# Kernel optimization log

Measured on AMD Instinct MI355X. Metric: run time of the kernel, lower is better.

## Reference

```python
import jax, jax.numpy as jnp
import numpy as np

B, CH, H, W = 32, 128, 32, 32
EMB = 64      # embedding_dim
NEMB = 8192   # codebook size


def setup_inputs() -> dict:
    key = jax.random.key(0)
    k1, k2, k3, k4 = jax.random.split(key, 4)
    z = jax.random.normal(k1, (B, CH, H, W), jnp.float32)
    # 1x1 conv == per-pixel linear: weight [EMB, CH], bias [EMB]
    proj_w = jax.random.normal(k2, (EMB, CH), jnp.float32) * 0.05
    proj_b = jax.random.normal(k3, (EMB,), jnp.float32) * 0.01
    embed_w = jax.random.normal(k4, (NEMB, EMB), jnp.float32)
    return {"z": z, "proj_w": proj_w, "proj_b": proj_b, "embed_w": embed_w}


def reference(z, proj_w, proj_b, embed_w):
    Bz, C, Hh, Ww = z.shape
    sg = jax.lax.stop_gradient
    # 1x1 conv then permute(0,2,3,1): [B,C,H,W] -> [B,H,W,E]
    z_e = jnp.einsum('bchw,ec->bhwe', z, proj_w) + proj_b
    flat = z_e.reshape(-1, z_e.shape[-1])  # [N, E], N = B*H*W
    dist = ((flat * flat).sum(1, keepdims=True)
            - 2.0 * (flat @ embed_w.T)
            + (embed_w * embed_w).sum(1)[None, :])
    z_q_ind = jnp.argmin(dist, axis=1).reshape(Bz, Hh, Ww)  # argmax(-dist)
    z_q_emb = embed_w[z_q_ind]  # gather: [B,H,W,E]
    commitment_cost = 0.25
    kld_scale = 10.0
    latent_loss = kld_scale * (
        commitment_cost * jnp.mean((sg(z_q_emb) - z_e) ** 2)
        + jnp.mean((z_q_emb - sg(z_e)) ** 2))
    z_q_flat = z_q_emb
    # straight-through estimator
    z_q_st = z_e + sg(z_q_emb - z_e)
    out = jnp.transpose(z_q_st, (0, 3, 1, 2))  # [B,E,H,W]
    return out, z_q_flat, latent_loss, z_q_ind
```

## Files before the change

kernel.cpp:

```cpp
#include <hip/hip_runtime.h>

#define NPIX   32768
#define NEMB_  8192
#define EMB_   64
#define CH_    128
#define CAPP   768

#define OUT_OFF  0
#define ZQ_OFF   2097152
#define LOSS_OFF 4194304
#define IND_OFF  4194305

typedef _Float16 h8   __attribute__((ext_vector_type(8)));
typedef float    f16f __attribute__((ext_vector_type(16)));

__global__ __launch_bounds__(256) void k_wpack(
    const float* __restrict__ ew, const float* __restrict__ pw,
    float4* __restrict__ W4, float* __restrict__ pwT,
    float* __restrict__ wsq, float* __restrict__ wsqp,
    float* __restrict__ lacc, int* __restrict__ done)
{
    const int tid = threadIdx.x;
    {
        const int i = blockIdx.x * 256 + tid;
        const float v = pw[i];
        const int e = i >> 7, c = i & 127;
        pwT[c * 64 + e] = v;
    }
    const int m = blockIdx.x * 256 + tid;
    const float4* wr = (const float4*)(ew + (size_t)m * EMB_);
    float w[EMB_];
    float s = 0.f;
    #pragma unroll
    for (int i = 0; i < 16; i++) {
        float4 v = wr[i];
        w[4*i] = v.x; w[4*i+1] = v.y; w[4*i+2] = v.z; w[4*i+3] = v.w;
        s += v.x*v.x + v.y*v.y + v.z*v.z + v.w*v.w;
    }
    wsq[m] = s;
    float sh = (float)(_Float16)s;
    float sl = s - sh;
    const int t  = m >> 5;
    const int li = m & 31;
    #pragma unroll
    for (int s5 = 0; s5 < 4; s5++) {
        #pragma unroll
        for (int h = 0; h < 2; h++) {
            h8 hh;
            #pragma unroll
            for (int j = 0; j < 8; j++) hh[j] = (_Float16)w[s5 * 16 + h * 8 + j];
            W4[(size_t)(t * 5 + s5) * 64 + h * 32 + li] = __builtin_bit_cast(float4, hh);
        }
    }
    {
        h8 hh;
        #pragma unroll
        for (int j = 0; j < 8; j++) hh[j] = (_Float16)0.f;
        hh[0] = (_Float16)sh; hh[1] = (_Float16)sl;
        W4[(size_t)(t * 5 + 4) * 64 + 0 * 32 + li] = __builtin_bit_cast(float4, hh);
        #pragma unroll
        for (int j = 0; j < 8; j++) hh[j] = (_Float16)0.f;
        W4[(size_t)(t * 5 + 4) * 64 + 1 * 32 + li] = __builtin_bit_cast(float4, hh);
    }
    __shared__ float red[256];
    red[tid] = s;
    __syncthreads();
    for (int o = 128; o > 0; o >>= 1) {
        if (tid < o) red[tid] = fmaxf(red[tid], red[tid + o]);
        __syncthreads();
    }
    if (tid == 0) wsqp[blockIdx.x] = red[0];
    if (blockIdx.x == 0 && tid == 0) { *lacc = 0.f; *done = 0; }
}

__global__ __launch_bounds__(256) void k_proj(
    const float* __restrict__ z, const float* __restrict__ pwT,
    const float* __restrict__ pb, float* __restrict__ z_e,
    float* __restrict__ xsq)
{
    __shared__ float xp[4][64];
    const int tid  = threadIdx.x;
    const int px   = tid & 63;
    const int eqv  = tid >> 6;
    const int eq16 = __builtin_amdgcn_readfirstlane(eqv << 4);
    const int n  = blockIdx.x * 64 + px;
    const int b  = n >> 10;
    const int hw = n & 1023;
    const float* zp = z + (size_t)b * (CH_ * 1024) + hw;

    float acc[16];
    #pragma unroll
    for (int j = 0; j < 16; j++) acc[j] = 0.f;

    #pragma unroll 4
    for (int c = 0; c < CH_; c++) {
        const float zv = zp[(size_t)c * 1024];
        const float4* wr = (const float4*)(pwT + c * 64 + eq16);
        float4 w0 = wr[0], w1 = wr[1], w2 = wr[2], w3 = wr[3];
        acc[0]  = fmaf(zv, w0.x, acc[0]);  acc[1]  = fmaf(zv, w0.y, acc[1]);
        acc[2]  = fmaf(zv, w0.z, acc[2]);  acc[3]  = fmaf(zv, w0.w, acc[3]);
        acc[4]  = fmaf(zv, w1.x, acc[4]);  acc[5]  = fmaf(zv, w1.y, acc[5]);
        acc[6]  = fmaf(zv, w1.z, acc[6]);  acc[7]  = fmaf(zv, w1.w, acc[7]);
        acc[8]  = fmaf(zv, w2.x, acc[8]);  acc[9]  = fmaf(zv, w2.y, acc[9]);
        acc[10] = fmaf(zv, w2.z, acc[10]); acc[11] = fmaf(zv, w2.w, acc[11]);
        acc[12] = fmaf(zv, w3.x, acc[12]); acc[13] = fmaf(zv, w3.y, acc[13]);
        acc[14] = fmaf(zv, w3.z, acc[14]); acc[15] = fmaf(zv, w3.w, acc[15]);
    }

    const float4* pb4 = (const float4*)(pb + eq16);
    float4 b0 = pb4[0], b1 = pb4[1], b2 = pb4[2], b3 = pb4[3];
    float bb[16] = {b0.x,b0.y,b0.z,b0.w, b1.x,b1.y,b1.z,b1.w,
                    b2.x,b2.y,b2.z,b2.w, b3.x,b3.y,b3.z,b3.w};
    float sq = 0.f;
    #pragma unroll
    for (int j = 0; j < 16; j++) { acc[j] += bb[j]; sq += acc[j] * acc[j]; }

    float4* zo = (float4*)(z_e + (size_t)n * EMB_ + eq16);
    zo[0] = make_float4(acc[0],  acc[1],  acc[2],  acc[3]);
    zo[1] = make_float4(acc[4],  acc[5],  acc[6],  acc[7]);
    zo[2] = make_float4(acc[8],  acc[9],  acc[10], acc[11]);
    zo[3] = make_float4(acc[12], acc[13], acc[14], acc[15]);
    xp[eqv][px] = sq;
    __syncthreads();
    if (tid < 64)
        xsq[blockIdx.x * 64 + tid] = xp[0][tid] + xp[1][tid] + xp[2][tid] + xp[3][tid];
}

__device__ __forceinline__ unsigned long long pack_key(float d, int m)
{
    unsigned fb = __float_as_uint(d);
    fb ^= ((int)fb < 0) ? 0xFFFFFFFFu : 0x80000000u;
    return ((unsigned long long)fb << 32) | (unsigned)m;
}

__global__ __launch_bounds__(512, 2) void k_fused3(
    const float4* __restrict__ W4, const float* __restrict__ z_e,
    const float* __restrict__ xsq, const float* __restrict__ wsqp,
    const float* __restrict__ wsq, const float* __restrict__ ew,
    float* __restrict__ out, float* __restrict__ lacc, int* __restrict__ done)
{
    __shared__ __align__(16) float xs[128][68];
    __shared__ float s1s[1024], s2s[1024], s3s[1024];
    __shared__ short i1s[1024], i2s[1024];
    __shared__ float thr_s[128];
    __shared__ int   pairs[CAPP];
    __shared__ unsigned long long pbest[128];
    __shared__ int   winner_s[128];
    __shared__ int   smask[128];
    __shared__ float wred[8];
    __shared__ int   npair_s;
    __shared__ float wm_s;

    const int tid  = threadIdx.x;
    const int wv   = tid >> 6;
    const int lane = tid & 63;
    const int n0   = blockIdx.x * 128;
    const int hlf  = lane >> 5;

    if (tid == 0) npair_s = 0;
    if (tid < 128) { smask[tid] = 0; pbest[tid] = ~0ULL; }
    if (tid < 32) {
        float w = wsqp[tid];
        #pragma unroll
        for (int o = 16; o > 0; o >>= 1) w = fmaxf(w, __shfl_xor(w, o));
        if (tid == 0) wm_s = w;
    }
    #pragma unroll
    for (int k = 0; k < 4; k++) {
        const int idx = k * 512 + tid;
        const int px = idx >> 4, i = idx & 15;
        ((float4*)&xs[px][0])[i] =
            *(const float4*)(z_e + (size_t)(n0 + px) * EMB_ + i * 4);
    }
    __syncthreads();

    h8 bfr[4][5];
    #pragma unroll
    for (int j = 0; j < 4; j++) {
        const int px = j * 32 + (lane & 31);
        #pragma unroll
        for (int s5 = 0; s5 < 4; s5++) {
            float4 u0 = *(const float4*)(&xs[px][s5 * 16 + hlf * 8]);
            float4 u1 = *(const float4*)(&xs[px][s5 * 16 + hlf * 8 + 4]);
            h8 hh;
            hh[0]=(_Float16)u0.x; hh[1]=(_Float16)u0.y; hh[2]=(_Float16)u0.z; hh[3]=(_Float16)u0.w;
            hh[4]=(_Float16)u1.x; hh[5]=(_Float16)u1.y; hh[6]=(_Float16)u1.z; hh[7]=(_Float16)u1.w;
            bfr[j][s5] = hh;
        }
        h8 hh;
        #pragma unroll
        for (int q = 0; q < 8; q++) hh[q] = (_Float16)0.f;
        if (hlf == 0) { hh[0] = (_Float16)-0.5f; hh[1] = (_Float16)-0.5f; }
        bfr[j][4] = hh;
    }

    const f16f kzero = {0,0,0,0,0,0,0,0,0,0,0,0,0,0,0,0};
    float s1[4], s2[4], s3[4];
    int   i1[4], i2[4];
    #pragma unroll
    for (int j = 0; j < 4; j++) { s1[j]=s2[j]=s3[j]=-3.0e38f; i1[j]=i2[j]=0; }

    const int tb = wv * 32;
    const float4* Wb = W4 + (size_t)tb * 320 + lane;
    float4 A0[5], A1[5];
    #pragma unroll
    for (int s = 0; s < 5; s++) A0[s] = Wb[s * 64];
    #pragma unroll
    for (int s = 0; s < 5; s++) A1[s] = Wb[320 + s * 64];

#define TILE_BODY(AB, TT, PF)                                                  \
    {                                                                          \
        const int gt = tb + (TT);                                              \
        f16f acc[4];                                                           \
        _Pragma("unroll")                                                      \
        for (int j = 0; j < 4; j++)                                            \
            acc[j] = __builtin_amdgcn_mfma_f32_32x32x16_f16(                   \
                __builtin_bit_cast(h8, AB[0]), bfr[j][0], kzero, 0, 0, 0);     \
        _Pragma("unroll")                                                      \
        for (int s = 1; s < 5; s++) {                                          \
            h8 a = __builtin_bit_cast(h8, AB[s]);                              \
            _Pragma("unroll")                                                  \
            for (int j = 0; j < 4; j++)                                        \
                acc[j] = __builtin_amdgcn_mfma_f32_32x32x16_f16(a, bfr[j][s],  \
                                                                acc[j],0,0,0); \
        }                                                                      \
        {                                                                      \
            const int tp = (PF) < 32 ? (PF) : 31;                              \
            const float4* wp = Wb + (size_t)tp * 320;                          \
            _Pragma("unroll")                                                  \
            for (int s = 0; s < 5; s++) AB[s] = wp[s * 64];                    \
        }                                                                      \
        _Pragma("unroll")                                                      \
        for (int j = 0; j < 4; j++) {                                          \
            float t0 = fmaxf(fmaxf(acc[j][0],  acc[j][1]),  acc[j][2]);        \
            float t1 = fmaxf(fmaxf(acc[j][3],  acc[j][4]),  acc[j][5]);        \
            float t2 = fmaxf(fmaxf(acc[j][6],  acc[j][7]),  acc[j][8]);        \
            float t3 = fmaxf(fmaxf(acc[j][9],  acc[j][10]), acc[j][11]);       \
            float t4 = fmaxf(fmaxf(acc[j][12], acc[j][13]), acc[j][14]);       \
            float v  = fmaxf(fmaxf(fmaxf(t0, t1), fmaxf(t2, t3)),              \
                             fmaxf(t4, acc[j][15]));                           \
            v = fmaxf(v, __shfl_xor(v, 32));                                   \
            bool c1 = v > s1[j];                                               \
            bool c2 = v > s2[j];                                               \
            int  cand = c1 ? i1[j] : gt;                                       \
            i2[j] = c2 ? cand : i2[j];                                         \
            s3[j] = fmaxf(fminf(s2[j], v), s3[j]);                             \
            s3[j] = fminf(s3[j], fmaxf(s2[j], v));                             \
            s2[j] = fmaxf(fminf(s1[j], v), fminf(s2[j], fmaxf(s1[j], v)));     \
            i1[j] = c1 ? gt : i1[j];                                           \
            s1[j] = fmaxf(s1[j], v);                                           \
        }                                                                      \
    }

    for (int tt = 0; tt < 32; tt += 2) {
        TILE_BODY(A0, tt,     tt + 2)
        TILE_BODY(A1, tt + 1, tt + 3)
    }
#undef TILE_BODY

    if (lane < 32) {
        #pragma unroll
        for (int j = 0; j < 4; j++) {
            const int cell = (j * 32 + lane) * 8 + wv;
            s1s[cell] = s1[j]; s2s[cell] = s2[j]; s3s[cell] = s3[j];
            i1s[cell] = (short)i1[j]; i2s[cell] = (short)i2[j];
        }
    }
    __syncthreads();

    if (tid < 128) {
        float s1g = s1s[tid * 8];
        #pragma unroll
        for (int c = 1; c < 8; c++) s1g = fmaxf(s1g, s1s[tid * 8 + c]);
        float E = 0.00125f * sqrtf(xsq[n0 + tid] * wm_s) + 1e-5f * wm_s + 3e-4f;
        thr_s[tid] = s1g - 2.0f * E;
    }
    __syncthreads();
    #pragma unroll
    for (int k = 0; k < 2; k++) {
        const int cell = k * 512 + tid;
        const int px = cell >> 3, ch = cell & 7;
        const float th = thr_s[px];
        const float cs1 = s1s[cell], cs2 = s2s[cell], cs3 = s3s[cell];
        if (cs3 >= th) {
            int pos = atomicAdd(&npair_s, 32);
            if (pos + 32 <= CAPP) {
                for (int t = 0; t < 32; t++)
                    pairs[pos + t] = (px << 8) | (ch * 32 + t);
            } else {
                for (int t = 0; t < 32; t++)
                    if (pos + t < CAPP) pairs[pos + t] = -1;
                smask[px] = 1;
            }
        } else {
            if (cs1 >= th) {
                int pos = atomicAdd(&npair_s, 1);
                if (pos < CAPP) pairs[pos] = (px << 8) | (int)i1s[cell];
                else smask[px] = 1;
            }
            if (cs2 >= th) {
                int pos = atomicAdd(&npair_s, 1);
                if (pos < CAPP) pairs[pos] = (px << 8) | (int)i2s[cell];
                else smask[px] = 1;
            }
        }
    }
    __syncthreads();
    const int np = npair_s < CAPP ? npair_s : CAPP;

    const int lg = lane >> 4;
    const int ld = lane & 15;
    for (int i = wv; i < np; i += 8) {
        const int pr = pairs[i];
        if (pr < 0) continue;
        const int p = pr >> 8;
        if (smask[p]) continue;
        const int t = pr & 255;
        const float4* tb4 = (const float4*)(ew + (size_t)t * 2048);
        float4 wq[8];
        #pragma unroll
        for (int q = 0; q < 8; q++) wq[q] = tb4[q * 64 + lane];
        const float4 xq = *(const float4*)(&xs[p][ld * 4]);
        unsigned long long best = ~0ULL;
        #pragma unroll
        for (int q = 0; q < 8; q++) {
            float dp = wq[q].x*xq.x + wq[q].y*xq.y + wq[q].z*xq.z + wq[q].w*xq.w;
            dp += __shfl_xor(dp, 1);
            dp += __shfl_xor(dp, 2);
            dp += __shfl_xor(dp, 4);
            dp += __shfl_xor(dp, 8);
            const int m = t * 32 + q * 4 + lg;
            unsigned long long key = pack_key(fmaf(-2.f, dp, wsq[m]), m);
            best = key < best ? key : best;
        }
        { unsigned long long o = __shfl_xor(best, 16); best = o < best ? o : best; }
        { unsigned long long o = __shfl_xor(best, 32); best = o < best ? o : best; }
        if (lane == 0) atomicMin(&pbest[p], best);
    }
    for (int p = wv; p < 128; p += 8) {
        if (!smask[p]) continue;
        const float4 xq = *(const float4*)(&xs[p][ld * 4]);
        unsigned long long bk = ~0ULL;
        for (int t = 0; t < 256; t++) {
            const float4* tb4 = (const float4*)(ew + (size_t)t * 2048);
            #pragma unroll
            for (int q = 0; q < 8; q++) {
                float4 wv4 = tb4[q * 64 + lane];
                float dp = wv4.x*xq.x + wv4.y*xq.y + wv4.z*xq.z + wv4.w*xq.w;
                dp += __shfl_xor(dp, 1);
                dp += __shfl_xor(dp, 2);
                dp += __shfl_xor(dp, 4);
                dp += __shfl_xor(dp, 8);
                const int m = t * 32 + q * 4 + lg;
                unsigned long long key = pack_key(fmaf(-2.f, dp, wsq[m]), m);
                bk = key < bk ? key : bk;
            }
        }
        { unsigned long long o = __shfl_xor(bk, 16); bk = o < bk ? o : bk; }
        { unsigned long long o = __shfl_xor(bk, 32); bk = o < bk ? o : bk; }
        if (lane == 0) atomicMin(&pbest[p], bk);
    }
    __syncthreads();
    if (tid < 128) {
        const int win = (int)(unsigned)(pbest[tid] & 0xFFFFFFFFULL);
        winner_s[tid] = win;
        out[IND_OFF + n0 + tid] = (float)win;
    }
    __syncthreads();
    float lsum = 0.f;
    {
        const int px = tid >> 2, sg = tid & 3;
        const int win = winner_s[px];
        const float4* wr = (const float4*)(ew + (size_t)win * EMB_ + sg * 16);
        float4* xr  = (float4*)(&xs[px][sg * 16]);
        float4* zq4 = (float4*)(out + ZQ_OFF + (size_t)(n0 + px) * EMB_ + sg * 16);
        #pragma unroll
        for (int i = 0; i < 4; i++) {
            float4 w4v = wr[i];
            float4 z4  = xr[i];
            float d0 = w4v.x - z4.x, d1 = w4v.y - z4.y;
            float d2 = w4v.z - z4.z, d3 = w4v.w - z4.w;
            lsum += d0*d0 + d1*d1 + d2*d2 + d3*d3;
            xr[i]  = w4v;
            zq4[i] = w4v;
        }
    }
    __syncthreads();
    {
        const int bI  = n0 >> 10;
        const int hw0 = n0 & 1023;
        float* ob = out + OUT_OFF + (size_t)bI * (EMB_ * 1024) + hw0;
        #pragma unroll
        for (int r = 0; r < 16; r++) {
            const int idx = r * 512 + tid;
            const int e = idx >> 7, px = idx & 127;
            ob[(size_t)e * 1024 + px] = xs[px][e];
        }
    }
    {
        float v = lsum;
        #pragma unroll
        for (int o = 1; o < 64; o <<= 1) v += __shfl_xor(v, o);
        if (lane == 0) wred[wv] = v;
    }
    __syncthreads();
    if (tid == 0) {
        float s = wred[0];
        #pragma unroll
        for (int k = 1; k < 8; k++) s += wred[k];
        atomicAdd(lacc, s);
        __threadfence();
        int old = atomicAdd(done, 1);
        if (old == (int)gridDim.x - 1) {
            float tot = atomicAdd(lacc, 0.0f);
            out[LOSS_OFF] = 12.5f * (tot / 2097152.0f);
        }
    }
}

extern "C" void kernel_launch(void* const* d_in, const int* in_sizes, int n_in,
                              void* d_out, int out_size, void* d_ws, size_t ws_size,
                              hipStream_t stream)
{
    const float* z  = (const float*)d_in[0];
    const float* pw = (const float*)d_in[1];
    const float* pb = (const float*)d_in[2];
    const float* ew = (const float*)d_in[3];
    float* out = (float*)d_out;

    char* ws = (char*)d_ws;
    float4* W4   = (float4*)(ws);
    float*  pwT  = (float*) (ws + 1310720);
    float*  xsq  = (float*) (ws + 1343488);
    float*  wsq  = (float*) (ws + 1474560);
    float*  wsqp = (float*) (ws + 1507328);
    float*  lacc = (float*) (ws + 1507456);
    int*    done = (int*)   (ws + 1507460);

    float* z_e = out + ZQ_OFF;

    hipLaunchKernelGGL(k_wpack,  dim3(32),  dim3(256), 0, stream,
                       ew, pw, W4, pwT, wsq, wsqp, lacc, done);
    hipLaunchKernelGGL(k_proj,   dim3(512), dim3(256), 0, stream,
                       z, pwT, pb, z_e, xsq);
    hipLaunchKernelGGL(k_fused3, dim3(256), dim3(512), 0, stream,
                       W4, z_e, xsq, wsqp, wsq, ew, out, lacc, done);
}
```

Baseline: 174.2 us.

## Fuse 1x1 projection into the VQ kernel and double threads per block

```diff
diff --git a/kernel.cpp b/kernel.cpp
--- a/kernel.cpp
+++ b/kernel.cpp
@@ -73,59 +73,6 @@
     if (blockIdx.x == 0 && tid == 0) { *lacc = 0.f; *done = 0; }
 }
 
-__global__ __launch_bounds__(256) void k_proj(
-    const float* __restrict__ z, const float* __restrict__ pwT,
-    const float* __restrict__ pb, float* __restrict__ z_e,
-    float* __restrict__ xsq)
-{
-    __shared__ float xp[4][64];
-    const int tid  = threadIdx.x;
-    const int px   = tid & 63;
-    const int eqv  = tid >> 6;
-    const int eq16 = __builtin_amdgcn_readfirstlane(eqv << 4);
-    const int n  = blockIdx.x * 64 + px;
-    const int b  = n >> 10;
-    const int hw = n & 1023;
-    const float* zp = z + (size_t)b * (CH_ * 1024) + hw;
-
-    float acc[16];
-    #pragma unroll
-    for (int j = 0; j < 16; j++) acc[j] = 0.f;
-
-    #pragma unroll 4
-    for (int c = 0; c < CH_; c++) {
-        const float zv = zp[(size_t)c * 1024];
-        const float4* wr = (const float4*)(pwT + c * 64 + eq16);
-        float4 w0 = wr[0], w1 = wr[1], w2 = wr[2], w3 = wr[3];
-        acc[0]  = fmaf(zv, w0.x, acc[0]);  acc[1]  = fmaf(zv, w0.y, acc[1]);
-        acc[2]  = fmaf(zv, w0.z, acc[2]);  acc[3]  = fmaf(zv, w0.w, acc[3]);
-        acc[4]  = fmaf(zv, w1.x, acc[4]);  acc[5]  = fmaf(zv, w1.y, acc[5]);
-        acc[6]  = fmaf(zv, w1.z, acc[6]);  acc[7]  = fmaf(zv, w1.w, acc[7]);
-        acc[8]  = fmaf(zv, w2.x, acc[8]);  acc[9]  = fmaf(zv, w2.y, acc[9]);
-        acc[10] = fmaf(zv, w2.z, acc[10]); acc[11] = fmaf(zv, w2.w, acc[11]);
-        acc[12] = fmaf(zv, w3.x, acc[12]); acc[13] = fmaf(zv, w3.y, acc[13]);
-        acc[14] = fmaf(zv, w3.z, acc[14]); acc[15] = fmaf(zv, w3.w, acc[15]);
-    }
-
-    const float4* pb4 = (const float4*)(pb + eq16);
-    float4 b0 = pb4[0], b1 = pb4[1], b2 = pb4[2], b3 = pb4[3];
-    float bb[16] = {b0.x,b0.y,b0.z,b0.w, b1.x,b1.y,b1.z,b1.w,
-                    b2.x,b2.y,b2.z,b2.w, b3.x,b3.y,b3.z,b3.w};
-    float sq = 0.f;
-    #pragma unroll
-    for (int j = 0; j < 16; j++) { acc[j] += bb[j]; sq += acc[j] * acc[j]; }
-
-    float4* zo = (float4*)(z_e + (size_t)n * EMB_ + eq16);
-    zo[0] = make_float4(acc[0],  acc[1],  acc[2],  acc[3]);
-    zo[1] = make_float4(acc[4],  acc[5],  acc[6],  acc[7]);
-    zo[2] = make_float4(acc[8],  acc[9],  acc[10], acc[11]);
-    zo[3] = make_float4(acc[12], acc[13], acc[14], acc[15]);
-    xp[eqv][px] = sq;
-    __syncthreads();
-    if (tid < 64)
-        xsq[blockIdx.x * 64 + tid] = xp[0][tid] + xp[1][tid] + xp[2][tid] + xp[3][tid];
-}
-
 __device__ __forceinline__ unsigned long long pack_key(float d, int m)
 {
     unsigned fb = __float_as_uint(d);
@@ -133,21 +80,23 @@
     return ((unsigned long long)fb << 32) | (unsigned)m;
 }
 
-__global__ __launch_bounds__(512, 2) void k_fused3(
-    const float4* __restrict__ W4, const float* __restrict__ z_e,
-    const float* __restrict__ xsq, const float* __restrict__ wsqp,
-    const float* __restrict__ wsq, const float* __restrict__ ew,
+__global__ __launch_bounds__(1024, 4) void k_fused3(
+    const float4* __restrict__ W4, const float* __restrict__ z,
+    const float* __restrict__ pwT, const float* __restrict__ pb,
+    const float* __restrict__ wsqp, const float* __restrict__ wsq,
+    const float* __restrict__ ew,
     float* __restrict__ out, float* __restrict__ lacc, int* __restrict__ done)
 {
     __shared__ __align__(16) float xs[128][68];
-    __shared__ float s1s[1024], s2s[1024], s3s[1024];
-    __shared__ short i1s[1024], i2s[1024];
+    __shared__ float s1s[2048], s2s[2048], s3s[2048];
+    __shared__ short i1s[2048], i2s[2048];
+    __shared__ float xsqp_s[8][128];
     __shared__ float thr_s[128];
     __shared__ int   pairs[CAPP];
     __shared__ unsigned long long pbest[128];
     __shared__ int   winner_s[128];
     __shared__ int   smask[128];
-    __shared__ float wred[8];
+    __shared__ float wred[16];
     __shared__ int   npair_s;
     __shared__ float wm_s;
 
@@ -165,12 +114,35 @@
         for (int o = 16; o > 0; o >>= 1) w = fmaxf(w, __shfl_xor(w, o));
         if (tid == 0) wm_s = w;
     }
-    #pragma unroll
-    for (int k = 0; k < 4; k++) {
-        const int idx = k * 512 + tid;
-        const int px = idx >> 4, i = idx & 15;
-        ((float4*)&xs[px][0])[i] =
-            *(const float4*)(z_e + (size_t)(n0 + px) * EMB_ + i * 4);
+
+    {
+        const int oct = tid >> 7;
+        const int pxp = tid & 127;
+        const int e0  = __builtin_amdgcn_readfirstlane(oct << 3);
+        const float* zp = z + (size_t)(n0 >> 10) * (CH_ * 1024) + (n0 & 1023) + pxp;
+        float acc[8];
+        #pragma unroll
+        for (int j = 0; j < 8; j++) acc[j] = 0.f;
+        #pragma unroll 8
+        for (int c = 0; c < CH_; c++) {
+            const float zv = zp[(size_t)c * 1024];
+            const float4* wr = (const float4*)(pwT + c * 64 + e0);
+            float4 w0 = wr[0], w1 = wr[1];
+            acc[0] = fmaf(zv, w0.x, acc[0]); acc[1] = fmaf(zv, w0.y, acc[1]);
+            acc[2] = fmaf(zv, w0.z, acc[2]); acc[3] = fmaf(zv, w0.w, acc[3]);
+            acc[4] = fmaf(zv, w1.x, acc[4]); acc[5] = fmaf(zv, w1.y, acc[5]);
+            acc[6] = fmaf(zv, w1.z, acc[6]); acc[7] = fmaf(zv, w1.w, acc[7]);
+        }
+        const float4* pb4 = (const float4*)(pb + e0);
+        float4 b0 = pb4[0], b1 = pb4[1];
+        acc[0] += b0.x; acc[1] += b0.y; acc[2] += b0.z; acc[3] += b0.w;
+        acc[4] += b1.x; acc[5] += b1.y; acc[6] += b1.z; acc[7] += b1.w;
+        float sq = 0.f;
+        #pragma unroll
+        for (int j = 0; j < 8; j++) sq += acc[j] * acc[j];
+        ((float4*)&xs[pxp][0])[oct * 2]     = make_float4(acc[0], acc[1], acc[2], acc[3]);
+        ((float4*)&xs[pxp][0])[oct * 2 + 1] = make_float4(acc[4], acc[5], acc[6], acc[7]);
+        xsqp_s[oct][pxp] = sq;
     }
     __syncthreads();
 
@@ -200,68 +172,72 @@
     #pragma unroll
     for (int j = 0; j < 4; j++) { s1[j]=s2[j]=s3[j]=-3.0e38f; i1[j]=i2[j]=0; }
 
-    const int tb = wv * 32;
+    const int tb = wv * 16;
     const float4* Wb = W4 + (size_t)tb * 320 + lane;
-    float4 A0[5], A1[5];
-    #pragma unroll
-    for (int s = 0; s < 5; s++) A0[s] = Wb[s * 64];
-    #pragma unroll
-    for (int s = 0; s < 5; s++) A1[s] = Wb[320 + s * 64];
-
-#define TILE_BODY(AB, TT, PF)                                                  \
+    float4 A[5];
+    #pragma unroll
+    for (int s = 0; s < 5; s++) A[s] = Wb[s * 64];
+
+#define REDUCE_J(ACC, JJ)                                                      \
     {                                                                          \
-        const int gt = tb + (TT);                                              \
-        f16f acc[4];                                                           \
-        _Pragma("unroll")                                                      \
-        for (int j = 0; j < 4; j++)                                            \
-            acc[j] = __builtin_amdgcn_mfma_f32_32x32x16_f16(                   \
-                __builtin_bit_cast(h8, AB[0]), bfr[j][0], kzero, 0, 0, 0);     \
-        _Pragma("unroll")                                                      \
-        for (int s = 1; s < 5; s++) {                                          \
-            h8 a = __builtin_bit_cast(h8, AB[s]);                              \
-            _Pragma("unroll")                                                  \
-            for (int j = 0; j < 4; j++)                                        \
-                acc[j] = __builtin_amdgcn_mfma_f32_32x32x16_f16(a, bfr[j][s],  \
-                                                                acc[j],0,0,0); \
-        }                                                                      \
-        {                                                                      \
-            const int tp = (PF) < 32 ? (PF) : 31;                              \
-            const float4* wp = Wb + (size_t)tp * 320;                          \
-            _Pragma("unroll")                                                  \
-            for (int s = 0; s < 5; s++) AB[s] = wp[s * 64];                    \
-        }                                                                      \
-        _Pragma("unroll")                                                      \
-        for (int j = 0; j < 4; j++) {                                          \
-            float t0 = fmaxf(fmaxf(acc[j][0],  acc[j][1]),  acc[j][2]);        \
-            float t1 = fmaxf(fmaxf(acc[j][3],  acc[j][4]),  acc[j][5]);        \
-            float t2 = fmaxf(fmaxf(acc[j][6],  acc[j][7]),  acc[j][8]);        \
-            float t3 = fmaxf(fmaxf(acc[j][9],  acc[j][10]), acc[j][11]);       \
-            float t4 = fmaxf(fmaxf(acc[j][12], acc[j][13]), acc[j][14]);       \
-            float v  = fmaxf(fmaxf(fmaxf(t0, t1), fmaxf(t2, t3)),              \
-                             fmaxf(t4, acc[j][15]));                           \
-            v = fmaxf(v, __shfl_xor(v, 32));                                   \
-            bool c1 = v > s1[j];                                               \
-            bool c2 = v > s2[j];                                               \
-            int  cand = c1 ? i1[j] : gt;                                       \
-            i2[j] = c2 ? cand : i2[j];                                         \
-            s3[j] = fmaxf(fminf(s2[j], v), s3[j]);                             \
-            s3[j] = fminf(s3[j], fmaxf(s2[j], v));                             \
-            s2[j] = fmaxf(fminf(s1[j], v), fminf(s2[j], fmaxf(s1[j], v)));     \
-            i1[j] = c1 ? gt : i1[j];                                           \
-            s1[j] = fmaxf(s1[j], v);                                           \
-        }                                                                      \
-    }
-
-    for (int tt = 0; tt < 32; tt += 2) {
-        TILE_BODY(A0, tt,     tt + 2)
-        TILE_BODY(A1, tt + 1, tt + 3)
-    }
-#undef TILE_BODY
+        float t0 = fmaxf(fmaxf(ACC[0],  ACC[1]),  ACC[2]);                     \
+        float t1 = fmaxf(fmaxf(ACC[3],  ACC[4]),  ACC[5]);                     \
+        float t2 = fmaxf(fmaxf(ACC[6],  ACC[7]),  ACC[8]);                     \
+        float t3 = fmaxf(fmaxf(ACC[9],  ACC[10]), ACC[11]);                    \
+        float t4 = fmaxf(fmaxf(ACC[12], ACC[13]), ACC[14]);                    \
+        float v  = fmaxf(fmaxf(fmaxf(t0, t1), fmaxf(t2, t3)),                  \
+                         fmaxf(t4, ACC[15]));                                  \
+        v = fmaxf(v, __shfl_xor(v, 32));                                       \
+        bool c1 = v > s1[JJ];                                                  \
+        bool c2 = v > s2[JJ];                                                  \
+        int  cand = c1 ? i1[JJ] : gt;                                          \
+        i2[JJ] = c2 ? cand : i2[JJ];                                           \
+        s3[JJ] = fmaxf(fminf(s2[JJ], v), s3[JJ]);                              \
+        s3[JJ] = fminf(s3[JJ], fmaxf(s2[JJ], v));                              \
+        s2[JJ] = fmaxf(fminf(s1[JJ], v), fminf(s2[JJ], fmaxf(s1[JJ], v)));     \
+        i1[JJ] = c1 ? gt : i1[JJ];                                             \
+        s1[JJ] = fmaxf(s1[JJ], v);                                             \
+    }
+
+    for (int tt = 0; tt < 16; tt++) {
+        const int gt = tb + tt;
+        f16f acc0 = __builtin_amdgcn_mfma_f32_32x32x16_f16(
+            __builtin_bit_cast(h8, A[0]), bfr[0][0], kzero, 0, 0, 0);
+        f16f acc1 = __builtin_amdgcn_mfma_f32_32x32x16_f16(
+            __builtin_bit_cast(h8, A[0]), bfr[1][0], kzero, 0, 0, 0);
+        #pragma unroll
+        for (int s = 1; s < 5; s++) {
+            h8 a = __builtin_bit_cast(h8, A[s]);
+            acc0 = __builtin_amdgcn_mfma_f32_32x32x16_f16(a, bfr[0][s], acc0, 0, 0, 0);
+            acc1 = __builtin_amdgcn_mfma_f32_32x32x16_f16(a, bfr[1][s], acc1, 0, 0, 0);
+        }
+        REDUCE_J(acc0, 0)
+        REDUCE_J(acc1, 1)
+        f16f acc2 = __builtin_amdgcn_mfma_f32_32x32x16_f16(
+            __builtin_bit_cast(h8, A[0]), bfr[2][0], kzero, 0, 0, 0);
+        f16f acc3 = __builtin_amdgcn_mfma_f32_32x32x16_f16(
+            __builtin_bit_cast(h8, A[0]), bfr[3][0], kzero, 0, 0, 0);
+        #pragma unroll
+        for (int s = 1; s < 5; s++) {
+            h8 a = __builtin_bit_cast(h8, A[s]);
+            acc2 = __builtin_amdgcn_mfma_f32_32x32x16_f16(a, bfr[2][s], acc2, 0, 0, 0);
+            acc3 = __builtin_amdgcn_mfma_f32_32x32x16_f16(a, bfr[3][s], acc3, 0, 0, 0);
+        }
+        {
+            const int tp = (tt + 1) < 16 ? (tt + 1) : 15;
+            const float4* wp = Wb + (size_t)tp * 320;
+            #pragma unroll
+            for (int s = 0; s < 5; s++) A[s] = wp[s * 64];
+        }
+        REDUCE_J(acc2, 2)
+        REDUCE_J(acc3, 3)
+    }
+#undef REDUCE_J
 
     if (lane < 32) {
         #pragma unroll
         for (int j = 0; j < 4; j++) {
-            const int cell = (j * 32 + lane) * 8 + wv;
+            const int cell = (j * 32 + lane) * 16 + wv;
             s1s[cell] = s1[j]; s2s[cell] = s2[j]; s3s[cell] = s3[j];
             i1s[cell] = (short)i1[j]; i2s[cell] = (short)i2[j];
         }
@@ -269,26 +245,29 @@
     __syncthreads();
 
     if (tid < 128) {
-        float s1g = s1s[tid * 8];
-        #pragma unroll
-        for (int c = 1; c < 8; c++) s1g = fmaxf(s1g, s1s[tid * 8 + c]);
-        float E = 0.00125f * sqrtf(xsq[n0 + tid] * wm_s) + 1e-5f * wm_s + 3e-4f;
+        float s1g = s1s[tid * 16];
+        #pragma unroll
+        for (int c = 1; c < 16; c++) s1g = fmaxf(s1g, s1s[tid * 16 + c]);
+        float xq = xsqp_s[0][tid];
+        #pragma unroll
+        for (int o = 1; o < 8; o++) xq += xsqp_s[o][tid];
+        float E = 0.00125f * sqrtf(xq * wm_s) + 1e-5f * wm_s + 3e-4f;
         thr_s[tid] = s1g - 2.0f * E;
     }
     __syncthreads();
     #pragma unroll
     for (int k = 0; k < 2; k++) {
-        const int cell = k * 512 + tid;
-        const int px = cell >> 3, ch = cell & 7;
+        const int cell = k * 1024 + tid;
+        const int px = cell >> 4, ch = cell & 15;
         const float th = thr_s[px];
         const float cs1 = s1s[cell], cs2 = s2s[cell], cs3 = s3s[cell];
         if (cs3 >= th) {
-            int pos = atomicAdd(&npair_s, 32);
-            if (pos + 32 <= CAPP) {
-                for (int t = 0; t < 32; t++)
-                    pairs[pos + t] = (px << 8) | (ch * 32 + t);
+            int pos = atomicAdd(&npair_s, 16);
+            if (pos + 16 <= CAPP) {
+                for (int t = 0; t < 16; t++)
+                    pairs[pos + t] = (px << 8) | (ch * 16 + t);
             } else {
-                for (int t = 0; t < 32; t++)
+                for (int t = 0; t < 16; t++)
                     if (pos + t < CAPP) pairs[pos + t] = -1;
                 smask[px] = 1;
             }
@@ -310,7 +289,7 @@
 
     const int lg = lane >> 4;
     const int ld = lane & 15;
-    for (int i = wv; i < np; i += 8) {
+    for (int i = wv; i < np; i += 16) {
         const int pr = pairs[i];
         if (pr < 0) continue;
         const int p = pr >> 8;
@@ -337,7 +316,7 @@
         { unsigned long long o = __shfl_xor(best, 32); best = o < best ? o : best; }
         if (lane == 0) atomicMin(&pbest[p], best);
     }
-    for (int p = wv; p < 128; p += 8) {
+    for (int p = wv; p < 128; p += 16) {
         if (!smask[p]) continue;
         const float4 xq = *(const float4*)(&xs[p][ld * 4]);
         unsigned long long bk = ~0ULL;
@@ -369,13 +348,13 @@
     __syncthreads();
     float lsum = 0.f;
     {
-        const int px = tid >> 2, sg = tid & 3;
+        const int px = tid >> 3, sg = tid & 7;
         const int win = winner_s[px];
-        const float4* wr = (const float4*)(ew + (size_t)win * EMB_ + sg * 16);
-        float4* xr  = (float4*)(&xs[px][sg * 16]);
-        float4* zq4 = (float4*)(out + ZQ_OFF + (size_t)(n0 + px) * EMB_ + sg * 16);
-        #pragma unroll
-        for (int i = 0; i < 4; i++) {
+        const float4* wr = (const float4*)(ew + (size_t)win * EMB_ + sg * 8);
+        float4* xr  = (float4*)(&xs[px][sg * 8]);
+        float4* zq4 = (float4*)(out + ZQ_OFF + (size_t)(n0 + px) * EMB_ + sg * 8);
+        #pragma unroll
+        for (int i = 0; i < 2; i++) {
             float4 w4v = wr[i];
             float4 z4  = xr[i];
             float d0 = w4v.x - z4.x, d1 = w4v.y - z4.y;
@@ -391,8 +370,8 @@
         const int hw0 = n0 & 1023;
         float* ob = out + OUT_OFF + (size_t)bI * (EMB_ * 1024) + hw0;
         #pragma unroll
-        for (int r = 0; r < 16; r++) {
-            const int idx = r * 512 + tid;
+        for (int r = 0; r < 8; r++) {
+            const int idx = r * 1024 + tid;
             const int e = idx >> 7, px = idx & 127;
             ob[(size_t)e * 1024 + px] = xs[px][e];
         }
@@ -407,7 +386,7 @@
     if (tid == 0) {
         float s = wred[0];
         #pragma unroll
-        for (int k = 1; k < 8; k++) s += wred[k];
+        for (int k = 1; k < 16; k++) s += wred[k];
         atomicAdd(lacc, s);
         __threadfence();
         int old = atomicAdd(done, 1);
@@ -431,18 +410,13 @@
     char* ws = (char*)d_ws;
     float4* W4   = (float4*)(ws);
     float*  pwT  = (float*) (ws + 1310720);
-    float*  xsq  = (float*) (ws + 1343488);
     float*  wsq  = (float*) (ws + 1474560);
     float*  wsqp = (float*) (ws + 1507328);
     float*  lacc = (float*) (ws + 1507456);
     int*    done = (int*)   (ws + 1507460);
 
-    float* z_e = out + ZQ_OFF;
-
     hipLaunchKernelGGL(k_wpack,  dim3(32),  dim3(256), 0, stream,
                        ew, pw, W4, pwT, wsq, wsqp, lacc, done);
-    hipLaunchKernelGGL(k_proj,   dim3(512), dim3(256), 0, stream,
-                       z, pwT, pb, z_e, xsq);
-    hipLaunchKernelGGL(k_fused3, dim3(256), dim3(512), 0, stream,
-                       W4, z_e, xsq, wsqp, wsq, ew, out, lacc, done);
+    hipLaunchKernelGGL(k_fused3, dim3(256), dim3(1024), 0, stream,
+                       W4, z, pwT, pb, wsqp, wsq, ew, out, lacc, done);
 }
```

After: 189.6 us. +8.9%, slower.
